# Kernel tuning notes

Measured on AMD Instinct MI355X. Metric: run time of the kernel, lower is better.

Reference implementation:

```python
import jax, jax.numpy as jnp
import numpy as np

BETA = 0.25
COMMIT_W = 1.0
EPS = 1e-6
N_E, E_DIM, C = 8192, 256, 256
B, H, W = 16, 32, 32


def setup_inputs() -> dict:
    key = jax.random.key(0)
    k1, k2, k3 = jax.random.split(key, 3)
    z = jax.random.normal(k1, (B, C, H, W), jnp.float32)
    frozen_codebook = jax.random.normal(k2, (N_E, E_DIM), jnp.float32) * (E_DIM ** -0.5)
    w_transform = jax.random.normal(k3, (C, E_DIM), jnp.float32) * (E_DIM ** -0.5)
    return {"z": z, "frozen_codebook": frozen_codebook, "w_transform": w_transform}


def _rotate_to(src, tgt):
    # Rotation trick: Householder-style rotation of src onto direction of tgt.
    sg = jax.lax.stop_gradient
    norm_src = jnp.linalg.norm(src, axis=-1, keepdims=True)
    norm_tgt = jnp.linalg.norm(tgt, axis=-1, keepdims=True)
    u = src / jnp.clip(norm_src, EPS)          # normalized source
    q = tgt / jnp.clip(norm_tgt, EPS)          # normalized target
    w = u + q
    w = sg(w / jnp.clip(jnp.linalg.norm(w, axis=-1, keepdims=True), EPS))
    u = sg(u)
    q = sg(q)
    e = src  # gradients flow through e only (rotation matrix is detached)
    rotated = (e
               - 2.0 * jnp.sum(e * w, axis=-1, keepdims=True) * w
               + 2.0 * jnp.sum(e * u, axis=-1, keepdims=True) * q)
    return rotated * sg(norm_tgt / jnp.clip(norm_src, EPS))


def reference(z, frozen_codebook, w_transform):
    z = z.astype(jnp.float32)
    zc = jnp.transpose(z, (0, 2, 3, 1))          # b h w c
    z_flat = zc.reshape(-1, zc.shape[-1])        # [N, C]
    codebook = frozen_codebook @ w_transform.T   # [n_e, C] (Linear, no bias)

    # squared L2 distances, argmin under no_grad
    d = (jnp.sum(z_flat ** 2, axis=1, keepdims=True)
         + jnp.sum(codebook ** 2, axis=1)
         - 2.0 * jnp.einsum('bd,nd->bn', z_flat, codebook))
    indices = jnp.argmin(jax.lax.stop_gradient(d), axis=1)  # [N]

    z_q_flat = codebook[indices]                 # [N, C]
    sg = jax.lax.stop_gradient
    loss = (jnp.mean((sg(z_flat) - z_q_flat) ** 2)
            + BETA * jnp.mean((z_flat - sg(z_q_flat)) ** 2)) * COMMIT_W

    z_q_flat = _rotate_to(z_flat, z_q_flat)      # rotation trick
    z_q = z_q_flat.reshape(zc.shape)             # b h w c
    z_q = jnp.transpose(z_q, (0, 3, 1, 2))       # b c h w
    return z_q, loss, indices
```

## Files before the change

### kernel.cpp

```cpp
#include <hip/hip_runtime.h>
#include <math.h>

typedef unsigned short u16;
typedef unsigned int   u32;

#define B_   16
#define C_   256
#define HW_  1024
#define N_   16384
#define NE_  8192
#define K_   256
#define NSPLIT 8
#define CPS  1024
#define NZQ  4194304

typedef _Float16 f16x8 __attribute__((ext_vector_type(8)));
typedef float    f32x16 __attribute__((ext_vector_type(16)));


__device__ __forceinline__ u16 f2h(float x) {
    union { _Float16 h; u16 u; } c;
    c.h = (_Float16)x;
    return c.u;
}

__global__ void k_transpose_z(const float* __restrict__ z, float* __restrict__ zf,
                              u16* __restrict__ zh) {
    __shared__ float tile[32][33];
    int b   = blockIdx.z;
    int hw0 = blockIdx.x * 32;
    int c0  = blockIdx.y * 32;
    int tx = threadIdx.x;
    int ty = threadIdx.y;
    #pragma unroll
    for (int i = 0; i < 4; ++i) {
        int c = c0 + ty + i * 8;
        tile[ty + i * 8][tx] = z[((size_t)b * C_ + c) * HW_ + hw0 + tx];
    }
    __syncthreads();
    #pragma unroll
    for (int i = 0; i < 4; ++i) {
        int hw = hw0 + ty + i * 8;
        size_t o = ((size_t)b * HW_ + hw) * C_ + c0 + tx;
        float v = tile[tx][ty + i * 8];
        zf[o] = v;
        zh[o] = f2h(v);
    }
}

__global__ __launch_bounds__(256) void k_codebook_gemm(
        const float* __restrict__ f, const float* __restrict__ w,
        float* __restrict__ cb, u16* __restrict__ cbh) {
    __shared__ float Fs[16][68];
    __shared__ float Ws[16][68];
    int n0 = blockIdx.x * 64;
    int c0 = blockIdx.y * 64;
    int tid = threadIdx.x;
    int tx = tid & 15, ty = tid >> 4;
    int nl = tid >> 2;
    int kq = (tid & 3) * 4;
    float acc[4][4] = {};
    for (int kb = 0; kb < K_; kb += 16) {
        float4 fv = *(const float4*)&f[(size_t)(n0 + nl) * K_ + kb + kq];
        float4 wv = *(const float4*)&w[(size_t)(c0 + nl) * K_ + kb + kq];
        __syncthreads();
        Fs[kq + 0][nl] = fv.x; Fs[kq + 1][nl] = fv.y; Fs[kq + 2][nl] = fv.z; Fs[kq + 3][nl] = fv.w;
        Ws[kq + 0][nl] = wv.x; Ws[kq + 1][nl] = wv.y; Ws[kq + 2][nl] = wv.z; Ws[kq + 3][nl] = wv.w;
        __syncthreads();
        #pragma unroll
        for (int k = 0; k < 16; ++k) {
            float4 a = *(float4*)&Fs[k][ty * 4];
            float4 b = *(float4*)&Ws[k][tx * 4];
            float av[4] = {a.x, a.y, a.z, a.w};
            float bv[4] = {b.x, b.y, b.z, b.w};
            #pragma unroll
            for (int i = 0; i < 4; ++i)
                #pragma unroll
                for (int j = 0; j < 4; ++j)
                    acc[i][j] += av[i] * bv[j];
        }
    }
    #pragma unroll
    for (int i = 0; i < 4; ++i) {
        size_t o = (size_t)(n0 + ty * 4 + i) * K_ + c0 + tx * 4;
        *(float4*)&cb[o] = make_float4(acc[i][0], acc[i][1], acc[i][2], acc[i][3]);
        *(ushort4*)&cbh[o] = make_ushort4(f2h(acc[i][0]), f2h(acc[i][1]),
                                          f2h(acc[i][2]), f2h(acc[i][3]));
    }
}

__global__ void k_c2(const float* __restrict__ cb, float* __restrict__ c2,
                     double* __restrict__ c2d) {
    int row  = blockIdx.x * 4 + (threadIdx.x >> 6);
    int lane = threadIdx.x & 63;
    float4 v = *(const float4*)&cb[(size_t)row * K_ + lane * 4];
    double s = (double)v.x * v.x + (double)v.y * v.y
             + (double)v.z * v.z + (double)v.w * v.w;
    #pragma unroll
    for (int off = 32; off; off >>= 1) s += __shfl_down(s, off, 64);
    if (lane == 0) { c2d[row] = s; c2[row] = (float)(s * 4096.0 + 262144.0); }
}

__device__ __forceinline__ void ld_lds16(const void* g, void* l) {
    __builtin_amdgcn_global_load_lds((const __attribute__((address_space(1))) void*)g,
                                     (__attribute__((address_space(3))) void*)l, 16, 0, 0);
}

#define INS(M1, M2, U) { u32 t_ = min(M1, U); u32 h_ = max(M1, U); M1 = t_; M2 = min(M2, h_); }

#define SCORE16(ACC, M1, M2, CGBASE, C2B) do {                                    \
    u32 ib_ = (u32)(code0 + (CGBASE));                                            \
    _Pragma("unroll")                                                             \
    for (int h = 0; h < 4; ++h) {                                                 \
        float4 cv = *(const float4*)&(C2B)[(CGBASE) + 8 * h];                     \
        u32 u0 = (((u32)fmaf(-8192.f, (ACC)[4*h+0], cv.x)) << 13) + ib_ + 8*h + 0; \
        u32 u1 = (((u32)fmaf(-8192.f, (ACC)[4*h+1], cv.y)) << 13) + ib_ + 8*h + 1; \
        u32 u2 = (((u32)fmaf(-8192.f, (ACC)[4*h+2], cv.z)) << 13) + ib_ + 8*h + 2; \
        u32 u3 = (((u32)fmaf(-8192.f, (ACC)[4*h+3], cv.w)) << 13) + ib_ + 8*h + 3; \
        INS(M1, M2, u0); INS(M1, M2, u1); INS(M1, M2, u2); INS(M1, M2, u3);       \
    }                                                                             \
} while (0)

__global__ __launch_bounds__(256, 2) void k_scan_mfma(
        const u16* __restrict__ zh, const u16* __restrict__ cbh,
        const float* __restrict__ c2, int* __restrict__ t2i) {
    __shared__ __align__(16) u16 sA[2][8192];
    __shared__ __align__(16) float c2s[2][128];

    int r0    = blockIdx.x * 128;
    int split = blockIdx.y;
    int tid  = threadIdx.x;
    int wave = tid >> 6, lane = tid & 63;
    int l31 = lane & 31, q = lane >> 5;
    int ra = ((wave & 1) << 6) + l31;

    const u16* zp = zh + (size_t)(r0 + ((wave >> 1) << 6) + l31) * K_ + q * 8;
    f16x8 zr0[16], zr1[16];
    #pragma unroll
    for (int t = 0; t < 16; ++t) {
        zr0[t] = *(const f16x8*)&zp[t * 16];
        zr1[t] = *(const f16x8*)&zp[32 * K_ + t * 16];
    }

    size_t ga[4]; u32 la[4];
    #pragma unroll
    for (int it = 0; it < 4; ++it) {
        int S = (it * 4 + wave) * 64 + lane;
        int row = S >> 3, u = S & 7;
        ga[it] = (size_t)row * K_ + (u ^ (row & 7)) * 8;
        la[it] = (u32)(it * 4 + wave) * 512;
    }

    u32 m1a = 0xFFFFFFFFu, m2a = 0xFFFFFFFFu;
    u32 m1b = 0xFFFFFFFFu, m2b = 0xFFFFFFFFu;

    const u16* cb0 = cbh + (size_t)split * CPS * K_;

    {
        #pragma unroll
        for (int it = 0; it < 4; ++it) ld_lds16(cb0 + ga[it], &sA[0][la[it]]);
        if (tid < 32) ld_lds16(&c2[split * CPS + tid * 4], &c2s[0][0]);
    }
    __syncthreads();

    f32x16 acc0 = (f32x16){}, acc1 = (f32x16){}, acc2 = (f32x16){}, acc3 = (f32x16){};
    for (int ct = 0; ct < 8; ++ct) {
        int code0 = split * CPS + ct * 128;
        const u16* Act = cb0 + (size_t)(ct * 128) * K_;
        #pragma unroll
        for (int kb = 0; kb < 4; ++kb) {
            if (kb < 3) {
                const u16* Ab = Act + (kb + 1) * 64;
                u16* d = &sA[(kb + 1) & 1][0];
                #pragma unroll
                for (int it = 0; it < 4; ++it) ld_lds16(Ab + ga[it], d + la[it]);
            } else if (ct < 7) {
                const u16* Ab = Act + (size_t)128 * K_;
                u16* d = &sA[0][0];
                #pragma unroll
                for (int it = 0; it < 4; ++it) ld_lds16(Ab + ga[it], d + la[it]);
                if (tid < 32) ld_lds16(&c2[code0 + 128 + tid * 4], &c2s[(ct + 1) & 1][0]);
            }
            const u16* sAb = &sA[kb & 1][0];
            __builtin_amdgcn_s_setprio(1);
            #pragma unroll
            for (int ks = 0; ks < 4; ++ks) {
                u32 u8 = (u32)(((ks * 2 + q) ^ (l31 & 7)) * 8);
                f16x8 af0 = *(const f16x8*)&sAb[(u32)ra * 64 + u8];
                f16x8 af1 = *(const f16x8*)&sAb[(u32)ra * 64 + 2048 + u8];
                acc0 = __builtin_amdgcn_mfma_f32_32x32x16_f16(af0, zr0[kb * 4 + ks], acc0, 0, 0, 0);
                acc1 = __builtin_amdgcn_mfma_f32_32x32x16_f16(af1, zr0[kb * 4 + ks], acc1, 0, 0, 0);
                acc2 = __builtin_amdgcn_mfma_f32_32x32x16_f16(af0, zr1[kb * 4 + ks], acc2, 0, 0, 0);
                acc3 = __builtin_amdgcn_mfma_f32_32x32x16_f16(af1, zr1[kb * 4 + ks], acc3, 0, 0, 0);
            }
            __builtin_amdgcn_s_setprio(0);
            if (kb == 3) {
                const float* C2B = &c2s[ct & 1][0];
                int cga = ((wave & 1) << 6) + (q << 2);
                int cgb = cga + 32;
                SCORE16(acc0, m1a, m2a, cga, C2B);
                SCORE16(acc1, m1a, m2a, cgb, C2B);
                SCORE16(acc2, m1b, m2b, cga, C2B);
                SCORE16(acc3, m1b, m2b, cgb, C2B);
                acc0 = (f32x16){}; acc1 = (f32x16){}; acc2 = (f32x16){}; acc3 = (f32x16){};
            }
            __syncthreads();
        }
    }

    {
        u32 o1 = __shfl_xor(m1a, 32, 64), o2 = __shfl_xor(m2a, 32, 64);
        u32 h = max(m1a, o1); m1a = min(m1a, o1); m2a = min(min(m2a, o2), h);
        o1 = __shfl_xor(m1b, 32, 64); o2 = __shfl_xor(m2b, 32, 64);
        h = max(m1b, o1); m1b = min(m1b, o1); m2b = min(min(m2b, o2), h);
    }
    u32* mbuf = (u32*)&sA[0][0];
    if (q == 0) {
        int base = ((wave * 2 + 0) * 32 + l31) * 2;
        mbuf[base] = m1a; mbuf[base + 1] = m2a;
        base = ((wave * 2 + 1) * 32 + l31) * 2;
        mbuf[base] = m1b; mbuf[base + 1] = m2b;
    }
    __syncthreads();
    if (tid < 128) {
        int zr = tid, wp = zr >> 6, zg = (zr >> 5) & 1, l = zr & 31;
        int iA = (((wp * 2 + 0) * 2 + zg) * 32 + l) * 2;
        int iB = (((wp * 2 + 1) * 2 + zg) * 32 + l) * 2;
        u32 a1 = mbuf[iA], a2 = mbuf[iA + 1];
        u32 b1 = mbuf[iB], b2 = mbuf[iB + 1];
        u32 h  = max(a1, b1), f1 = min(a1, b1);
        u32 f2 = min(min(a2, b2), h);
        size_t o = ((size_t)split * N_ + (r0 + zr)) * 2;
        t2i[o] = (int)(f1 & 0x1FFFu);
        t2i[o + 1] = (int)(f2 & 0x1FFFu);
    }
}

__global__ __launch_bounds__(256) void k_finalize(
        const float* __restrict__ zf, const float* __restrict__ cb,
        const double* __restrict__ c2d, const int* __restrict__ t2i,
        float* __restrict__ out, float* __restrict__ partials) {
    __shared__ int   bidx[16];
    __shared__ float wsum[4];
    __shared__ float tile[16][260];
    int n0 = blockIdx.x * 16;
    int tid = threadIdx.x;
    int wv = tid >> 6, lane = tid & 63;
    int h = lane >> 5, l5 = lane & 31;

    for (int rr = 0; rr < 4; ++rr) {
        int n = n0 + wv * 4 + rr;
        double bs = 1e300; int bi = 0x7fffffff;
        for (int p = 0; p < 8; ++p) {
            int t = 2 * p + h;
            int sp = t >> 1, wsel = t & 1;
            int ci = t2i[((size_t)sp * N_ + n) * 2 + wsel];
            double acc = 0.0;
            const float* zp = zf + (size_t)n * K_;
            const float* cp = cb + (size_t)ci * K_;
            #pragma unroll
            for (int jj = 0; jj < 2; ++jj) {
                float4 zv = *(const float4*)&zp[l5 * 4 + jj * 128];
                float4 cv = *(const float4*)&cp[l5 * 4 + jj * 128];
                acc += (double)zv.x * cv.x + (double)zv.y * cv.y
                     + (double)zv.z * cv.z + (double)zv.w * cv.w;
            }
            #pragma unroll
            for (int off = 1; off < 32; off <<= 1) acc += __shfl_xor(acc, off, 32);
            double sc = c2d[ci] - 2.0 * acc;
            double so = __shfl_xor(sc, 32, 64);
            int    io = __shfl_xor(ci, 32, 64);
            double s0 = h ? so : sc;  int i0 = h ? io : ci;
            double s1 = h ? sc : so;  int i1 = h ? ci : io;
            if (s0 < bs || (s0 == bs && i0 < bi)) { bs = s0; bi = i0; }
            if (s1 < bs || (s1 == bs && i1 < bi)) { bs = s1; bi = i1; }
        }
        if (lane == 0) {
            bidx[wv * 4 + rr] = bi;
            out[(size_t)NZQ + 1 + n] = (float)bi;
        }
    }
    __syncthreads();

    float accl = 0.f;
    for (int l = 0; l < 16; ++l) {
        int n = n0 + l;
        int bi = bidx[l];
        float zq = cb[(size_t)bi * K_ + tid];
        float d  = zf[(size_t)n * K_ + tid] - zq;
        accl += d * d;
        tile[l][tid] = zq;
    }
    #pragma unroll
    for (int off = 32; off; off >>= 1) accl += __shfl_down(accl, off, 64);
    if ((tid & 63) == 0) wsum[tid >> 6] = accl;
    __syncthreads();
    if (tid == 0) partials[blockIdx.x] = wsum[0] + wsum[1] + wsum[2] + wsum[3];
    int b = n0 >> 10, hw0 = n0 & 1023;
    #pragma unroll
    for (int g = 0; g < 4; ++g) {
        float4 v = make_float4(tile[g * 4 + 0][tid], tile[g * 4 + 1][tid],
                               tile[g * 4 + 2][tid], tile[g * 4 + 3][tid]);
        *(float4*)&out[((size_t)b * C_ + tid) * HW_ + hw0 + g * 4] = v;
    }
}

__global__ void k_loss(const float* __restrict__ partials, float* __restrict__ out) {
    __shared__ double ws4[4];
    int tid = threadIdx.x;
    double s = 0.0;
    for (int i = tid; i < 1024; i += 256) s += (double)partials[i];
    #pragma unroll
    for (int off = 32; off; off >>= 1) s += __shfl_down(s, off, 64);
    if ((tid & 63) == 0) ws4[tid >> 6] = s;
    __syncthreads();
    if (tid == 0) {
        double tot = ws4[0] + ws4[1] + ws4[2] + ws4[3];
        out[NZQ] = (float)(1.25 * tot / (double)NZQ);
    }
}

extern "C" void kernel_launch(void* const* d_in, const int* in_sizes, int n_in,
                              void* d_out, int out_size, void* d_ws, size_t ws_size,
                              hipStream_t stream) {
    const float* z  = (const float*)d_in[0];
    const float* fc = (const float*)d_in[1];
    const float* wt = (const float*)d_in[2];
    float* out = (float*)d_out;

    float* ws = (float*)d_ws;
    const size_t OFF_ZF   = 0;
    const size_t OFF_CB   = OFF_ZF + (size_t)N_ * K_;
    const size_t OFF_C2   = OFF_CB + (size_t)NE_ * K_;
    const size_t OFF_C2D  = OFF_C2 + NE_;
    const size_t OFF_T2I  = OFF_C2D + (size_t)NE_ * 2;
    const size_t OFF_PART = OFF_T2I + (size_t)NSPLIT * N_ * 2;
    const size_t OFF_ZH   = OFF_PART + 1024;
    const size_t OFF_CBH  = OFF_ZH + (size_t)N_ * K_ / 2;

    float*  zf   = ws + OFF_ZF;
    float*  cb   = ws + OFF_CB;
    float*  c2   = ws + OFF_C2;
    double* c2d  = (double*)(ws + OFF_C2D);
    int*    t2i  = (int*)(ws + OFF_T2I);
    float*  part = ws + OFF_PART;
    u16*    zh   = (u16*)(ws + OFF_ZH);
    u16*    cbh  = (u16*)(ws + OFF_CBH);

    k_transpose_z<<<dim3(HW_ / 32, C_ / 32, B_), dim3(32, 8), 0, stream>>>(z, zf, zh);
    k_codebook_gemm<<<dim3(NE_ / 64, K_ / 64), 256, 0, stream>>>(fc, wt, cb, cbh);
    k_c2<<<NE_ / 4, 256, 0, stream>>>(cb, c2, c2d);
    k_scan_mfma<<<dim3(N_ / 128, NSPLIT), 256, 0, stream>>>(zh, cbh, c2, t2i);
    k_finalize<<<N_ / 16, 256, 0, stream>>>(zf, cb, c2d, t2i, out, part);
    k_loss<<<1, 256, 0, stream>>>(part, out);
}
```

Baseline: 226.3 us.

## Deepen codebook LDS pipeline to four-buffer ring with explicit vmcnt waits

The codebook tile staging moves from a two-buffer scheme to a four-slot LDS ring with a prefetch distance of two stages. Per-step `__syncthreads` is replaced by an explicit `s_waitcnt vmcnt` plus a single `s_barrier`. All 1024 c2 norms for the split are loaded into LDS once up front instead of being double-buffered per code tile. The goal is more time for global-to-LDS loads to land behind the MFMA work and less synchronization stall. In exchange, LDS use per block roughly doubles, which could limit occupancy at two blocks per CU.

```diff
diff --git a/kernel.cpp b/kernel.cpp
--- a/kernel.cpp
+++ b/kernel.cpp
@@ -121,11 +121,15 @@
     }                                                                             \
 } while (0)
 
+#define WAITVM(N) { asm volatile("s_waitcnt vmcnt(" #N ")" ::: "memory"); \
+                    __builtin_amdgcn_s_barrier();                          \
+                    __builtin_amdgcn_sched_barrier(0); }
+
 __global__ __launch_bounds__(256, 2) void k_scan_mfma(
         const u16* __restrict__ zh, const u16* __restrict__ cbh,
         const float* __restrict__ c2, int* __restrict__ t2i) {
-    __shared__ __align__(16) u16 sA[2][8192];
-    __shared__ __align__(16) float c2s[2][128];
+    __shared__ __align__(16) u16 sA[4][8192];
+    __shared__ __align__(16) float c2s[1024];
 
     int r0    = blockIdx.x * 128;
     int split = blockIdx.y;
@@ -156,57 +160,60 @@
 
     const u16* cb0 = cbh + (size_t)split * CPS * K_;
 
-    {
+    auto STAGE = [&](int s) {
+        const u16* Ab = cb0 + (size_t)(s >> 2) * (128 * K_) + (s & 3) * 64;
+        u16* d = &sA[s & 3][0];
         #pragma unroll
-        for (int it = 0; it < 4; ++it) ld_lds16(cb0 + ga[it], &sA[0][la[it]]);
-        if (tid < 32) ld_lds16(&c2[split * CPS + tid * 4], &c2s[0][0]);
-    }
-    __syncthreads();
+        for (int it = 0; it < 4; ++it) ld_lds16(Ab + ga[it], d + la[it]);
+    };
 
     f32x16 acc0 = (f32x16){}, acc1 = (f32x16){}, acc2 = (f32x16){}, acc3 = (f32x16){};
-    for (int ct = 0; ct < 8; ++ct) {
-        int code0 = split * CPS + ct * 128;
-        const u16* Act = cb0 + (size_t)(ct * 128) * K_;
+
+    auto COMPUTE = [&](int ct, int kb) {
+        const u16* sAb = &sA[kb][0];
+        __builtin_amdgcn_s_setprio(1);
+        #pragma unroll
+        for (int ks = 0; ks < 4; ++ks) {
+            u32 u8 = (u32)(((ks * 2 + q) ^ (l31 & 7)) * 8);
+            f16x8 af0 = *(const f16x8*)&sAb[(u32)ra * 64 + u8];
+            f16x8 af1 = *(const f16x8*)&sAb[(u32)ra * 64 + 2048 + u8];
+            acc0 = __builtin_amdgcn_mfma_f32_32x32x16_f16(af0, zr0[kb * 4 + ks], acc0, 0, 0, 0);
+            acc1 = __builtin_amdgcn_mfma_f32_32x32x16_f16(af1, zr0[kb * 4 + ks], acc1, 0, 0, 0);
+            acc2 = __builtin_amdgcn_mfma_f32_32x32x16_f16(af0, zr1[kb * 4 + ks], acc2, 0, 0, 0);
+            acc3 = __builtin_amdgcn_mfma_f32_32x32x16_f16(af1, zr1[kb * 4 + ks], acc3, 0, 0, 0);
+        }
+        __builtin_amdgcn_s_setprio(0);
+        if (kb == 3) {
+            int code0 = split * CPS + ct * 128;
+            const float* C2B = &c2s[ct * 128];
+            int cga = ((wave & 1) << 6) + (q << 2);
+            int cgb = cga + 32;
+            SCORE16(acc0, m1a, m2a, cga, C2B);
+            SCORE16(acc1, m1a, m2a, cgb, C2B);
+            SCORE16(acc2, m1b, m2b, cga, C2B);
+            SCORE16(acc3, m1b, m2b, cgb, C2B);
+            acc0 = (f32x16){}; acc1 = (f32x16){}; acc2 = (f32x16){}; acc3 = (f32x16){};
+        }
+    };
+
+    STAGE(0); STAGE(1);
+    ld_lds16(&c2[split * CPS + wave * 256 + lane * 4], &c2s[wave * 256]);
+    asm volatile("s_waitcnt vmcnt(0)" ::: "memory");
+    __builtin_amdgcn_s_barrier();
+    __builtin_amdgcn_sched_barrier(0);
+
+    for (int ct = 0; ct < 7; ++ct) {
         #pragma unroll
         for (int kb = 0; kb < 4; ++kb) {
-            if (kb < 3) {
-                const u16* Ab = Act + (kb + 1) * 64;
-                u16* d = &sA[(kb + 1) & 1][0];
-                #pragma unroll
-                for (int it = 0; it < 4; ++it) ld_lds16(Ab + ga[it], d + la[it]);
-            } else if (ct < 7) {
-                const u16* Ab = Act + (size_t)128 * K_;
-                u16* d = &sA[0][0];
-                #pragma unroll
-                for (int it = 0; it < 4; ++it) ld_lds16(Ab + ga[it], d + la[it]);
-                if (tid < 32) ld_lds16(&c2[code0 + 128 + tid * 4], &c2s[(ct + 1) & 1][0]);
-            }
-            const u16* sAb = &sA[kb & 1][0];
-            __builtin_amdgcn_s_setprio(1);
-            #pragma unroll
-            for (int ks = 0; ks < 4; ++ks) {
-                u32 u8 = (u32)(((ks * 2 + q) ^ (l31 & 7)) * 8);
-                f16x8 af0 = *(const f16x8*)&sAb[(u32)ra * 64 + u8];
-                f16x8 af1 = *(const f16x8*)&sAb[(u32)ra * 64 + 2048 + u8];
-                acc0 = __builtin_amdgcn_mfma_f32_32x32x16_f16(af0, zr0[kb * 4 + ks], acc0, 0, 0, 0);
-                acc1 = __builtin_amdgcn_mfma_f32_32x32x16_f16(af1, zr0[kb * 4 + ks], acc1, 0, 0, 0);
-                acc2 = __builtin_amdgcn_mfma_f32_32x32x16_f16(af0, zr1[kb * 4 + ks], acc2, 0, 0, 0);
-                acc3 = __builtin_amdgcn_mfma_f32_32x32x16_f16(af1, zr1[kb * 4 + ks], acc3, 0, 0, 0);
-            }
-            __builtin_amdgcn_s_setprio(0);
-            if (kb == 3) {
-                const float* C2B = &c2s[ct & 1][0];
-                int cga = ((wave & 1) << 6) + (q << 2);
-                int cgb = cga + 32;
-                SCORE16(acc0, m1a, m2a, cga, C2B);
-                SCORE16(acc1, m1a, m2a, cgb, C2B);
-                SCORE16(acc2, m1b, m2b, cga, C2B);
-                SCORE16(acc3, m1b, m2b, cgb, C2B);
-                acc0 = (f32x16){}; acc1 = (f32x16){}; acc2 = (f32x16){}; acc3 = (f32x16){};
-            }
-            __syncthreads();
-        }
-    }
+            STAGE(ct * 4 + kb + 2);
+            WAITVM(8);
+            COMPUTE(ct, kb);
+        }
+    }
+    STAGE(30); WAITVM(8); COMPUTE(7, 0);
+    STAGE(31); WAITVM(8); COMPUTE(7, 1);
+    WAITVM(4);            COMPUTE(7, 2);
+    WAITVM(0);            COMPUTE(7, 3);
 
     {
         u32 o1 = __shfl_xor(m1a, 32, 64), o2 = __shfl_xor(m2a, 32, 64);
```

Result: no change. 224.3 us (-0.9%).
